# Kernel tuning notes

Hardware: AMD Instinct MI355X
Metric: run time of the kernel (lower is better)

Reference implementation:

```python
import jax, jax.numpy as jnp
import numpy as np

VOCAB = 23
PAD_IDX = 21
SOS_IDX = 22
LATENT = 128
COND = 16
HID = 1024
EMB = 512
MAX_LEN = 64
B = 4096


def setup_inputs() -> dict:
    key = jax.random.key(0)
    ks = jax.random.split(key, 12)
    s = lambda *d: 1.0 / np.sqrt(d[-1])
    inp = {
        "z": jax.random.normal(ks[0], (B, LATENT), jnp.float32),
        "cond": jax.random.normal(ks[1], (B, COND), jnp.float32),
        "emb_table": jax.random.normal(ks[2], (VOCAB, EMB), jnp.float32),
        "W_lh": jax.random.uniform(ks[3], (HID, LATENT + COND), jnp.float32, -s(LATENT + COND), s(LATENT + COND)),
        "b_lh": jax.random.uniform(ks[4], (HID,), jnp.float32, -s(LATENT + COND), s(LATENT + COND)),
        "W_ih": jax.random.uniform(ks[5], (4 * HID, EMB), jnp.float32, -s(HID), s(HID)),
        "W_hh": jax.random.uniform(ks[6], (4 * HID, HID), jnp.float32, -s(HID), s(HID)),
        "b_ih": jax.random.uniform(ks[7], (4 * HID,), jnp.float32, -s(HID), s(HID)),
        "b_hh": jax.random.uniform(ks[8], (4 * HID,), jnp.float32, -s(HID), s(HID)),
        "W_out": jax.random.uniform(ks[9], (VOCAB, HID), jnp.float32, -s(HID), s(HID)),
        "b_out": jax.random.uniform(ks[10], (VOCAB,), jnp.float32, -s(HID), s(HID)),
    }
    return inp


def reference(z, cond, emb_table, W_lh, b_lh, W_ih, W_hh, b_ih, b_hh, W_out, b_out):
    # padding_idx row of the embedding is zero (and non-trainable in torch)
    E = emb_table.at[PAD_IDX].set(0.0)
    # initial hidden from latent+cond; initial cell is zeros
    h0 = jnp.concatenate([z, cond], axis=1) @ W_lh.T + b_lh          # [B, H]
    c0 = jnp.zeros_like(h0)
    x0 = E[jnp.full((z.shape[0],), SOS_IDX, dtype=jnp.int32)]        # [B, E]
    bias = b_ih + b_hh

    def step(carry, _):
        h, c, x = carry
        gates = x @ W_ih.T + h @ W_hh.T + bias                        # [B, 4H]
        i, f, g, o = jnp.split(gates, 4, axis=1)
        i = jax.nn.sigmoid(i)
        f = jax.nn.sigmoid(f)
        g = jnp.tanh(g)
        o = jax.nn.sigmoid(o)
        c = f * c + i * g
        h = o * jnp.tanh(c)
        logits = h @ W_out.T + b_out                                  # [B, V]
        nxt = jnp.argmax(logits, axis=1)                              # greedy token
        x = E[nxt]
        return (h, c, x), logits

    _, logits_t = jax.lax.scan(step, (h0, c0, x0), None, length=MAX_LEN)  # [T, B, V]
    return jnp.transpose(logits_t, (1, 0, 2))                         # [B, T, V]
```

## Files before the change

kernel.cpp:

```cpp
#include <hip/hip_runtime.h>

#define NB 4096
#define NH 1024
#define NE 512
#define NV 23
#define NT 64
#define NL 144
#define PADV 21
#define SOSV 22

typedef unsigned short u16;
typedef __attribute__((ext_vector_type(4))) float f32x4;
typedef __attribute__((ext_vector_type(8))) __bf16 bf16x8;
typedef __attribute__((ext_vector_type(8))) unsigned short u16x8;

__device__ __forceinline__ u16 f2bf(float x) {
  unsigned u = __float_as_uint(x);
  u += 0x7FFFu + ((u >> 16) & 1u);
  return (u16)(u >> 16);
}
__device__ __forceinline__ float bf2f(u16 h) {
  return __uint_as_float(((unsigned)h) << 16);
}

__device__ __forceinline__ size_t hidx(int m, int j) {
  return ((size_t)(((m >> 8) * 32 + (j >> 5)) * 4 + ((j >> 3) & 3)) * 2048)
         + (size_t)((m & 255) * 8) + (j & 7);
}

__global__ void prep_kernel(const float* __restrict__ Whh, u16* __restrict__ Whi,
                            u16* __restrict__ Wlo, float* __restrict__ c,
                            int* __restrict__ tok) {
  int i = blockIdx.x * 256 + threadIdx.x;
  float wv = Whh[i];
  u16 hi = f2bf(wv);
  u16 lo = f2bf(wv - bf2f(hi));
  const int nw = i >> 10, k = i & 1023;
  const int g = nw >> 10, jcol = nw & 1023;
  const int jt = jcol >> 6, jl = jcol & 63;
  const int row = g * 64 + jl;
  const size_t oi = ((size_t)((jt * 32 + (k >> 5)) * 4 + ((k >> 3) & 3)) * 2048)
                    + (size_t)(row * 8) + (k & 7);
  Whi[oi] = hi;
  Wlo[oi] = lo;
  c[i] = 0.0f;
  if (i < NB) tok[i] = SOSV;
}

__global__ void exw_kernel(const float* __restrict__ emb, const float* __restrict__ Wih,
                           const float* __restrict__ bih, const float* __restrict__ bhh,
                           float* __restrict__ ExW) {
  __shared__ float Es[NE];
  const int v = blockIdx.y;
  const int n = blockIdx.x * 256 + threadIdx.x;
  for (int k = threadIdx.x; k < NE; k += 256)
    Es[k] = (v == PADV) ? 0.0f : emb[v * NE + k];
  __syncthreads();
  float s = bih[n] + bhh[n];
  const float* wr = Wih + (long)n * NE;
  for (int k = 0; k < NE; ++k) s = fmaf(Es[k], wr[k], s);
  ExW[v * (4 * NH) + n] = s;
}

__global__ void h0_kernel(const float* __restrict__ z, const float* __restrict__ cnd,
                          const float* __restrict__ Wlh, const float* __restrict__ blh,
                          u16* __restrict__ hhi, u16* __restrict__ hlo) {
  __shared__ float zc[8][NL];
  const int b0 = blockIdx.y * 8;
  const int j = blockIdx.x * 256 + threadIdx.x;
  for (int idx = threadIdx.x; idx < 8 * NL; idx += 256) {
    int bi = idx / NL, k = idx % NL;
    zc[bi][k] = (k < 128) ? z[(long)(b0 + bi) * 128 + k]
                          : cnd[(long)(b0 + bi) * 16 + (k - 128)];
  }
  __syncthreads();
  float acc[8];
  const float bj = blh[j];
#pragma unroll
  for (int bi = 0; bi < 8; ++bi) acc[bi] = bj;
  const float* wr = Wlh + (long)j * NL;
  for (int k = 0; k < NL; ++k) {
    float wv = wr[k];
#pragma unroll
    for (int bi = 0; bi < 8; ++bi) acc[bi] = fmaf(wv, zc[bi][k], acc[bi]);
  }
#pragma unroll
  for (int bi = 0; bi < 8; ++bi) {
    size_t idx = hidx(b0 + bi, j);
    u16 hi = f2bf(acc[bi]);
    hhi[idx] = hi;
    hlo[idx] = f2bf(acc[bi] - bf2f(hi));
  }
}

__device__ __forceinline__ void gll(const u16* src, u16* dst) {
  __builtin_amdgcn_global_load_lds(
      (const __attribute__((address_space(1))) void*)src,
      (__attribute__((address_space(3))) void*)dst, 16, 0, 0);
}

__global__ __launch_bounds__(256, 2)
void gates_cell_kernel(const u16* __restrict__ Whi, const u16* __restrict__ Wlo,
                       const u16* __restrict__ hhi_in, const u16* __restrict__ hlo_in,
                       const float* __restrict__ ExW, const int* __restrict__ tok,
                       float* __restrict__ c, u16* __restrict__ hhi_out,
                       u16* __restrict__ hlo_out) {
  __shared__ u16 lds[32768];

  const int bid = blockIdx.x;
  const int swz = (bid & 7) * 64 + (bid >> 3);
  const int jt = swz >> 5;
  const int bm = swz & 31;
  const int m0 = bm << 7;
  const int j0 = jt << 6;

  const int tid = threadIdx.x;
  const int w = tid >> 6, l = tid & 63;
  const int wm = w >> 1, wn = w & 1;
  const int q = l >> 4, rL = l & 15;

  const int smat = w >> 1, shalf = w & 1;
  const u16* simg = smat ? Wlo : Whi;
  const size_t sB = (size_t)jt * 262144 + (size_t)shalf * 4096 + (size_t)l * 8;
  u16* sdst0 = (u16*)lds + smat * 8192 + shalf * 4096 + l * 8;

  const int slab = bm >> 1;
  const int arow0 = ((bm & 1) << 7) + wm * 64 + rL;
  const size_t aBase = ((size_t)slab * 128 + q) * 2048 + (size_t)arow0 * 8;

  f32x4 acc[4][8];
#pragma unroll
  for (int mi = 0; mi < 4; ++mi)
#pragma unroll
    for (int ni = 0; ni < 8; ++ni) acc[mi][ni] = (f32x4){0.f, 0.f, 0.f, 0.f};

  bf16x8 A0h[4], A0l[4], A1h[4], A1l[4];

#pragma unroll
  for (int i = 0; i < 8; ++i) gll(simg + sB + i * 512, sdst0 + i * 512);
#pragma unroll
  for (int mi = 0; mi < 4; ++mi) {
    A0h[mi] = *reinterpret_cast<const bf16x8*>(hhi_in + aBase + mi * 128);
    A0l[mi] = *reinterpret_cast<const bf16x8*>(hlo_in + aBase + mi * 128);
  }
  __syncthreads();

  auto body = [&](int ks, int buf, bf16x8* aCh, bf16x8* aCl,
                  bf16x8* aNh, bf16x8* aNl) {
    if (ks < 31) {
      const u16* src = simg + sB + (size_t)(ks + 1) * 8192;
      u16* dst = sdst0 + (buf ^ 1) * 16384;
#pragma unroll
      for (int i = 0; i < 8; ++i) gll(src + i * 512, dst + i * 512);
      const size_t ao = aBase + (size_t)(ks + 1) * 8192;
#pragma unroll
      for (int mi = 0; mi < 4; ++mi) {
        aNh[mi] = *reinterpret_cast<const bf16x8*>(hhi_in + ao + mi * 128);
        aNl[mi] = *reinterpret_cast<const bf16x8*>(hlo_in + ao + mi * 128);
      }
    }
    const u16* bb = lds + buf * 16384;
#pragma unroll
    for (int ni = 0; ni < 2; ++ni) {
#pragma unroll
      for (int g = 0; g < 4; ++g) {
        const int ro = q * 2048 + (g * 64 + wn * 32 + ni * 16 + rL) * 8;
        const bf16x8 bh = *reinterpret_cast<const bf16x8*>(bb + ro);
        const bf16x8 bl = *reinterpret_cast<const bf16x8*>(bb + 8192 + ro);
        const int ai = g * 2 + ni;
#pragma unroll
        for (int mi = 0; mi < 4; ++mi)
          acc[mi][ai] = __builtin_amdgcn_mfma_f32_16x16x32_bf16(aCh[mi], bh, acc[mi][ai], 0, 0, 0);
#pragma unroll
        for (int mi = 0; mi < 4; ++mi)
          acc[mi][ai] = __builtin_amdgcn_mfma_f32_16x16x32_bf16(aCh[mi], bl, acc[mi][ai], 0, 0, 0);
#pragma unroll
        for (int mi = 0; mi < 4; ++mi)
          acc[mi][ai] = __builtin_amdgcn_mfma_f32_16x16x32_bf16(aCl[mi], bh, acc[mi][ai], 0, 0, 0);
      }
    }
    __syncthreads();
  };

  for (int ks2 = 0; ks2 < 32; ks2 += 2) {
    body(ks2, 0, A0h, A0l, A1h, A1l);
    body(ks2 + 1, 1, A1h, A1l, A0h, A0l);
  }

#pragma unroll
  for (int mi = 0; mi < 4; ++mi) {
#pragma unroll
    for (int r = 0; r < 4; ++r) {
      const int m = m0 + wm * 64 + mi * 16 + q * 4 + r;
      const int tk = tok[m];
      const float* exr = ExW + (size_t)tk * 4096;
#pragma unroll
      for (int ni = 0; ni < 2; ++ni) {
        const int j = j0 + wn * 32 + ni * 16 + rL;
        const float gi = acc[mi][0 * 2 + ni][r] + exr[j];
        const float gf = acc[mi][1 * 2 + ni][r] + exr[NH + j];
        const float gg = acc[mi][2 * 2 + ni][r] + exr[2 * NH + j];
        const float go = acc[mi][3 * 2 + ni][r] + exr[3 * NH + j];
        const float i_ = 1.0f / (1.0f + expf(-gi));
        const float f_ = 1.0f / (1.0f + expf(-gf));
        const float g_ = tanhf(gg);
        const float o_ = 1.0f / (1.0f + expf(-go));
        const size_t cidx = (size_t)m * NH + j;
        const float cn = f_ * c[cidx] + i_ * g_;
        c[cidx] = cn;
        const float hn = o_ * tanhf(cn);
        const u16 hi = f2bf(hn);
        const size_t oidx = hidx(m, j);
        hhi_out[oidx] = hi;
        hlo_out[oidx] = f2bf(hn - bf2f(hi));
      }
    }
  }
}

__global__ __launch_bounds__(256)
void logits_kernel(const u16* __restrict__ hhi, const u16* __restrict__ hlo,
                   const float* __restrict__ Wout, const float* __restrict__ bout,
                   float* __restrict__ out, int* __restrict__ tok, int t) {
  __shared__ float hs[8][NH];
  __shared__ float part[8][24][8];
  __shared__ float lg[8][24];
  const int b0 = blockIdx.x * 8;
  const int tid = threadIdx.x;
  for (int ci = tid; ci < 1024; ci += 256) {
    const int bi = ci >> 7, cj = ci & 127;
    const int m = b0 + bi;
    const int ks = cj >> 2, qq = cj & 3;
    const size_t base = ((size_t)(((m >> 8) * 32 + ks) * 4 + qq) * 2048)
                        + (size_t)((m & 255) * 8);
    const u16x8 vh = *reinterpret_cast<const u16x8*>(hhi + base);
    const u16x8 vl = *reinterpret_cast<const u16x8*>(hlo + base);
    const int kb = ks * 32 + qq * 8;
#pragma unroll
    for (int e = 0; e < 8; ++e) hs[bi][kb + e] = bf2f(vh[e]) + bf2f(vl[e]);
  }
  __syncthreads();
  const int v = tid & 31, kc = tid >> 5;
  if (v < NV) {
    float s[8];
#pragma unroll
    for (int bi = 0; bi < 8; ++bi) s[bi] = 0.f;
    const float* wr = Wout + (long)v * NH + kc * 128;
    const int kb = kc * 128;
    for (int k = 0; k < 128; ++k) {
      float wv = wr[k];
#pragma unroll
      for (int bi = 0; bi < 8; ++bi) s[bi] = fmaf(wv, hs[bi][kb + k], s[bi]);
    }
#pragma unroll
    for (int bi = 0; bi < 8; ++bi) part[kc][v][bi] = s[bi];
  }
  __syncthreads();
  if (tid < NV * 8) {
    const int vv = tid >> 3, bi = tid & 7;
    float s = bout[vv];
#pragma unroll
    for (int k = 0; k < 8; ++k) s += part[k][vv][bi];
    lg[bi][vv] = s;
    out[((long)(b0 + bi) * NT + t) * NV + vv] = s;
  }
  __syncthreads();
  if (tid < 8) {
    float best = lg[tid][0];
    int bv = 0;
    for (int vv = 1; vv < NV; ++vv) {
      float x = lg[tid][vv];
      if (x > best) { best = x; bv = vv; }
    }
    tok[b0 + tid] = bv;
  }
}

extern "C" void kernel_launch(void* const* d_in, const int* in_sizes, int n_in,
                              void* d_out, int out_size, void* d_ws, size_t ws_size,
                              hipStream_t stream) {
  const float* z    = (const float*)d_in[0];
  const float* cnd  = (const float*)d_in[1];
  const float* emb  = (const float*)d_in[2];
  const float* Wlh  = (const float*)d_in[3];
  const float* blh  = (const float*)d_in[4];
  const float* Wih  = (const float*)d_in[5];
  const float* Whh  = (const float*)d_in[6];
  const float* bih  = (const float*)d_in[7];
  const float* bhh  = (const float*)d_in[8];
  const float* Wout = (const float*)d_in[9];
  const float* bout = (const float*)d_in[10];
  float* out = (float*)d_out;

  char* ws = (char*)d_ws;
  size_t off = 0;
  auto alloc = [&](size_t bytes) -> void* {
    off = (off + 255) & ~(size_t)255;
    void* p = ws + off;
    off += bytes;
    return p;
  };
  u16* Whi = (u16*)alloc((size_t)4 * NH * NH * 2);
  u16* Wlo = (u16*)alloc((size_t)4 * NH * NH * 2);
  float* ExW = (float*)alloc((size_t)NV * 4 * NH * 4);
  u16* hhi0 = (u16*)alloc((size_t)NB * NH * 2);
  u16* hhi1 = (u16*)alloc((size_t)NB * NH * 2);
  u16* hlo0 = (u16*)alloc((size_t)NB * NH * 2);
  u16* hlo1 = (u16*)alloc((size_t)NB * NH * 2);
  float* cbuf = (float*)alloc((size_t)NB * NH * 4);
  int* tokb = (int*)alloc((size_t)NB * 4);
  u16* hhi[2] = {hhi0, hhi1};
  u16* hlo[2] = {hlo0, hlo1};

  prep_kernel<<<dim3((4 * NH * NH) / 256), dim3(256), 0, stream>>>(Whh, Whi, Wlo, cbuf, tokb);
  exw_kernel<<<dim3((4 * NH) / 256, NV), dim3(256), 0, stream>>>(emb, Wih, bih, bhh, ExW);
  h0_kernel<<<dim3(NH / 256, NB / 8), dim3(256), 0, stream>>>(z, cnd, Wlh, blh, hhi[0], hlo[0]);

  int p = 0;
  for (int t = 0; t < NT; ++t) {
    gates_cell_kernel<<<dim3(512), dim3(256), 0, stream>>>(
        Whi, Wlo, hhi[p], hlo[p], ExW, tokb, cbuf, hhi[p ^ 1], hlo[p ^ 1]);
    logits_kernel<<<dim3(NB / 8), dim3(256), 0, stream>>>(
        hhi[p ^ 1], hlo[p ^ 1], Wout, bout, out, tokb, t);
    p ^= 1;
  }
}
```

Measured before the change: 6.871 ms.

## Shrink gates tile to 128x32 columns, stage both h and W through LDS

The gates kernel now uses 128-row by 32-hidden-column tiles (1024 blocks instead of 512), with the hidden state and weight blocking changed to 128-row/32-column slabs. Both the A operand (h hi/lo) and the B operand (W hi/lo) are loaded into LDS with global_load_lds by separate waves, replacing the direct-to-register A loads. The block-to-tile mapping groups four column tiles per XCD so the L2 can reuse weights, and tokens are prefetched before the main loop. This buys more blocks and fewer accumulator registers per thread, at the cost of less data reuse per tile and extra LDS traffic for A.

After: 6.815 ms. About the same (-0.8%).

```diff
diff --git a/kernel.cpp b/kernel.cpp
--- a/kernel.cpp
+++ b/kernel.cpp
@@ -24,8 +24,8 @@
 }
 
 __device__ __forceinline__ size_t hidx(int m, int j) {
-  return ((size_t)(((m >> 8) * 32 + (j >> 5)) * 4 + ((j >> 3) & 3)) * 2048)
-         + (size_t)((m & 255) * 8) + (j & 7);
+  return ((size_t)(((m >> 7) * 32 + (j >> 5)) * 4 + ((j >> 3) & 3)) * 1024)
+         + (size_t)((m & 127) * 8) + (j & 7);
 }
 
 __global__ void prep_kernel(const float* __restrict__ Whh, u16* __restrict__ Whi,
@@ -37,9 +37,9 @@
   u16 lo = f2bf(wv - bf2f(hi));
   const int nw = i >> 10, k = i & 1023;
   const int g = nw >> 10, jcol = nw & 1023;
-  const int jt = jcol >> 6, jl = jcol & 63;
-  const int row = g * 64 + jl;
-  const size_t oi = ((size_t)((jt * 32 + (k >> 5)) * 4 + ((k >> 3) & 3)) * 2048)
+  const int jt = jcol >> 5, jl = jcol & 31;
+  const int row = (g << 5) + jl;
+  const size_t oi = ((size_t)((jt * 32 + (k >> 5)) * 4 + ((k >> 3) & 3)) * 1024)
                     + (size_t)(row * 8) + (k & 7);
   Whi[oi] = hi;
   Wlo[oi] = lo;
@@ -108,112 +108,98 @@
   __shared__ u16 lds[32768];
 
   const int bid = blockIdx.x;
-  const int swz = (bid & 7) * 64 + (bid >> 3);
-  const int jt = swz >> 5;
-  const int bm = swz & 31;
-  const int m0 = bm << 7;
-  const int j0 = jt << 6;
+  const int xcd = bid & 7;
+  const int local = bid >> 3;
+  const int jt = (xcd << 2) | (local & 3);
+  const int mt = local >> 2;
+  const int m0 = mt << 7;
+  const int j0 = jt << 5;
 
   const int tid = threadIdx.x;
   const int w = tid >> 6, l = tid & 63;
   const int wm = w >> 1, wn = w & 1;
   const int q = l >> 4, rL = l & 15;
 
-  const int smat = w >> 1, shalf = w & 1;
-  const u16* simg = smat ? Wlo : Whi;
-  const size_t sB = (size_t)jt * 262144 + (size_t)shalf * 4096 + (size_t)l * 8;
-  u16* sdst0 = (u16*)lds + smat * 8192 + shalf * 4096 + l * 8;
-
-  const int slab = bm >> 1;
-  const int arow0 = ((bm & 1) << 7) + wm * 64 + rL;
-  const size_t aBase = ((size_t)slab * 128 + q) * 2048 + (size_t)arow0 * 8;
-
-  f32x4 acc[4][8];
+  const u16* simg = (w == 0) ? hhi_in : (w == 1) ? hlo_in : (w == 2) ? Whi : Wlo;
+  const size_t sbase = ((w < 2) ? ((size_t)mt * 131072) : ((size_t)jt * 131072))
+                       + (size_t)l * 8;
+  const u16* sit = simg + sbase;
+  u16* dwave = (u16*)lds + w * 8192 + l * 8;
+
+  int tkv[16];
 #pragma unroll
   for (int mi = 0; mi < 4; ++mi)
 #pragma unroll
-    for (int ni = 0; ni < 8; ++ni) acc[mi][ni] = (f32x4){0.f, 0.f, 0.f, 0.f};
-
-  bf16x8 A0h[4], A0l[4], A1h[4], A1l[4];
-
-#pragma unroll
-  for (int i = 0; i < 8; ++i) gll(simg + sB + i * 512, sdst0 + i * 512);
-#pragma unroll
-  for (int mi = 0; mi < 4; ++mi) {
-    A0h[mi] = *reinterpret_cast<const bf16x8*>(hhi_in + aBase + mi * 128);
-    A0l[mi] = *reinterpret_cast<const bf16x8*>(hlo_in + aBase + mi * 128);
-  }
-  __syncthreads();
-
-  auto body = [&](int ks, int buf, bf16x8* aCh, bf16x8* aCl,
-                  bf16x8* aNh, bf16x8* aNl) {
+    for (int r = 0; r < 4; ++r)
+      tkv[mi * 4 + r] = tok[m0 + wm * 64 + mi * 16 + q * 4 + r];
+
+  f32x4 acc[4][4];
+#pragma unroll
+  for (int mi = 0; mi < 4; ++mi)
+#pragma unroll
+    for (int g = 0; g < 4; ++g) acc[mi][g] = (f32x4){0.f, 0.f, 0.f, 0.f};
+
+#pragma unroll
+  for (int i = 0; i < 8; ++i) gll(sit + i * 512, dwave + i * 512);
+  __syncthreads();
+
+  for (int ks = 0; ks < 32; ++ks) {
+    const int buf = ks & 1;
     if (ks < 31) {
-      const u16* src = simg + sB + (size_t)(ks + 1) * 8192;
-      u16* dst = sdst0 + (buf ^ 1) * 16384;
+      const u16* src = sit + (size_t)(ks + 1) * 4096;
+      u16* dst = dwave + (buf ^ 1) * 4096;
 #pragma unroll
       for (int i = 0; i < 8; ++i) gll(src + i * 512, dst + i * 512);
-      const size_t ao = aBase + (size_t)(ks + 1) * 8192;
-#pragma unroll
-      for (int mi = 0; mi < 4; ++mi) {
-        aNh[mi] = *reinterpret_cast<const bf16x8*>(hhi_in + ao + mi * 128);
-        aNl[mi] = *reinterpret_cast<const bf16x8*>(hlo_in + ao + mi * 128);
-      }
-    }
-    const u16* bb = lds + buf * 16384;
-#pragma unroll
-    for (int ni = 0; ni < 2; ++ni) {
-#pragma unroll
-      for (int g = 0; g < 4; ++g) {
-        const int ro = q * 2048 + (g * 64 + wn * 32 + ni * 16 + rL) * 8;
-        const bf16x8 bh = *reinterpret_cast<const bf16x8*>(bb + ro);
-        const bf16x8 bl = *reinterpret_cast<const bf16x8*>(bb + 8192 + ro);
-        const int ai = g * 2 + ni;
-#pragma unroll
-        for (int mi = 0; mi < 4; ++mi)
-          acc[mi][ai] = __builtin_amdgcn_mfma_f32_16x16x32_bf16(aCh[mi], bh, acc[mi][ai], 0, 0, 0);
-#pragma unroll
-        for (int mi = 0; mi < 4; ++mi)
-          acc[mi][ai] = __builtin_amdgcn_mfma_f32_16x16x32_bf16(aCh[mi], bl, acc[mi][ai], 0, 0, 0);
-#pragma unroll
-        for (int mi = 0; mi < 4; ++mi)
-          acc[mi][ai] = __builtin_amdgcn_mfma_f32_16x16x32_bf16(aCl[mi], bh, acc[mi][ai], 0, 0, 0);
-      }
+    }
+    const u16* base = lds + buf * 4096 + q * 1024;
+    bf16x8 ah[4], al[4];
+#pragma unroll
+    for (int mi = 0; mi < 4; ++mi) {
+      const int ao = (wm * 64 + mi * 16 + rL) * 8;
+      ah[mi] = *reinterpret_cast<const bf16x8*>(base + ao);
+      al[mi] = *reinterpret_cast<const bf16x8*>(base + 8192 + ao);
+    }
+#pragma unroll
+    for (int g = 0; g < 4; ++g) {
+      const int bo = (g * 32 + wn * 16 + rL) * 8;
+      const bf16x8 bh = *reinterpret_cast<const bf16x8*>(base + 16384 + bo);
+      const bf16x8 bl = *reinterpret_cast<const bf16x8*>(base + 24576 + bo);
+#pragma unroll
+      for (int mi = 0; mi < 4; ++mi)
+        acc[mi][g] = __builtin_amdgcn_mfma_f32_16x16x32_bf16(ah[mi], bh, acc[mi][g], 0, 0, 0);
+#pragma unroll
+      for (int mi = 0; mi < 4; ++mi)
+        acc[mi][g] = __builtin_amdgcn_mfma_f32_16x16x32_bf16(ah[mi], bl, acc[mi][g], 0, 0, 0);
+#pragma unroll
+      for (int mi = 0; mi < 4; ++mi)
+        acc[mi][g] = __builtin_amdgcn_mfma_f32_16x16x32_bf16(al[mi], bh, acc[mi][g], 0, 0, 0);
     }
     __syncthreads();
-  };
-
-  for (int ks2 = 0; ks2 < 32; ks2 += 2) {
-    body(ks2, 0, A0h, A0l, A1h, A1l);
-    body(ks2 + 1, 1, A1h, A1l, A0h, A0l);
-  }
-
+  }
+
+  const int j = j0 + wn * 16 + rL;
 #pragma unroll
   for (int mi = 0; mi < 4; ++mi) {
 #pragma unroll
     for (int r = 0; r < 4; ++r) {
       const int m = m0 + wm * 64 + mi * 16 + q * 4 + r;
-      const int tk = tok[m];
-      const float* exr = ExW + (size_t)tk * 4096;
-#pragma unroll
-      for (int ni = 0; ni < 2; ++ni) {
-        const int j = j0 + wn * 32 + ni * 16 + rL;
-        const float gi = acc[mi][0 * 2 + ni][r] + exr[j];
-        const float gf = acc[mi][1 * 2 + ni][r] + exr[NH + j];
-        const float gg = acc[mi][2 * 2 + ni][r] + exr[2 * NH + j];
-        const float go = acc[mi][3 * 2 + ni][r] + exr[3 * NH + j];
-        const float i_ = 1.0f / (1.0f + expf(-gi));
-        const float f_ = 1.0f / (1.0f + expf(-gf));
-        const float g_ = tanhf(gg);
-        const float o_ = 1.0f / (1.0f + expf(-go));
-        const size_t cidx = (size_t)m * NH + j;
-        const float cn = f_ * c[cidx] + i_ * g_;
-        c[cidx] = cn;
-        const float hn = o_ * tanhf(cn);
-        const u16 hi = f2bf(hn);
-        const size_t oidx = hidx(m, j);
-        hhi_out[oidx] = hi;
-        hlo_out[oidx] = f2bf(hn - bf2f(hi));
-      }
+      const float* exr = ExW + (size_t)tkv[mi * 4 + r] * 4096;
+      const float gi = acc[mi][0][r] + exr[j];
+      const float gf = acc[mi][1][r] + exr[NH + j];
+      const float gg = acc[mi][2][r] + exr[2 * NH + j];
+      const float go = acc[mi][3][r] + exr[3 * NH + j];
+      const float i_ = 1.0f / (1.0f + expf(-gi));
+      const float f_ = 1.0f / (1.0f + expf(-gf));
+      const float g_ = tanhf(gg);
+      const float o_ = 1.0f / (1.0f + expf(-go));
+      const size_t cidx = (size_t)m * NH + j;
+      const float cn = f_ * c[cidx] + i_ * g_;
+      c[cidx] = cn;
+      const float hn = o_ * tanhf(cn);
+      const u16 hi = f2bf(hn);
+      const size_t oidx = hidx(m, j);
+      hhi_out[oidx] = hi;
+      hlo_out[oidx] = f2bf(hn - bf2f(hi));
     }
   }
 }
@@ -231,8 +217,8 @@
     const int bi = ci >> 7, cj = ci & 127;
     const int m = b0 + bi;
     const int ks = cj >> 2, qq = cj & 3;
-    const size_t base = ((size_t)(((m >> 8) * 32 + ks) * 4 + qq) * 2048)
-                        + (size_t)((m & 255) * 8);
+    const size_t base = ((size_t)(((m >> 7) * 32 + ks) * 4 + qq) * 1024)
+                        + (size_t)((m & 127) * 8);
     const u16x8 vh = *reinterpret_cast<const u16x8*>(hhi + base);
     const u16x8 vl = *reinterpret_cast<const u16x8*>(hlo + base);
     const int kb = ks * 32 + qq * 8;
@@ -318,7 +304,7 @@
 
   int p = 0;
   for (int t = 0; t < NT; ++t) {
-    gates_cell_kernel<<<dim3(512), dim3(256), 0, stream>>>(
+    gates_cell_kernel<<<dim3(1024), dim3(256), 0, stream>>>(
         Whi, Wlo, hhi[p], hlo[p], ExW, tokb, cbuf, hhi[p ^ 1], hlo[p ^ 1]);
     logits_kernel<<<dim3(NB / 8), dim3(256), 0, stream>>>(
         hhi[p ^ 1], hlo[p ^ 1], Wout, bout, out, tokb, t);
```
